# Kernel optimization log

Measured on AMD Instinct MI355X. Metric: run time of the kernel, lower is better.

The kernel has to match this reference:

```python
import jax, jax.numpy as jnp
import numpy as np

B, S, D = 4, 2048, 1024
H, DK, DV = 16, 64, 64


def setup_inputs() -> dict:
    key = jax.random.key(0)
    ks = jax.random.split(key, 9)
    std = 1.0 / np.sqrt(D)
    inp = {
        "x": jax.random.normal(ks[0], (B, S, D), jnp.float32),
        "c": jax.random.normal(ks[1], (B, S, D), jnp.float32),
        "Wq_x": jax.random.normal(ks[2], (D, H * DK), jnp.float32) * std,
        "Wk_x": jax.random.normal(ks[3], (D, H * DK), jnp.float32) * std,
        "Wv_x": jax.random.normal(ks[4], (D, H * DV), jnp.float32) * std,
        "Wq_c": jax.random.normal(ks[5], (D, H * DK), jnp.float32) * std,
        "Wk_c": jax.random.normal(ks[6], (D, H * DK), jnp.float32) * std,
        "Wv_c": jax.random.normal(ks[7], (D, H * DV), jnp.float32) * std,
        "W_proj": jax.random.normal(ks[8], (2 * H * DV, D), jnp.float32) * (1.0 / np.sqrt(2 * H * DV)),
        "b_proj": jnp.zeros((D,), jnp.float32),
    }
    return inp


def _heads(t, hd):
    # [B,S,H*hd] -> [B,H,S,hd]
    b, s, _ = t.shape
    return t.reshape(b, s, H, hd).transpose(0, 2, 1, 3)


def reference(x, c, Wq_x, Wk_x, Wv_x, Wq_c, Wk_c, Wv_c, W_proj, b_proj):
    q = jnp.concatenate([_heads(x @ Wq_x, DK), _heads(c @ Wq_c, DK)], axis=-1)  # [B,H,S,2DK]
    k = jnp.concatenate([_heads(x @ Wk_x, DK), _heads(c @ Wk_c, DK)], axis=-1)
    v = jnp.concatenate([_heads(x @ Wv_x, DV), _heads(c @ Wv_c, DV)], axis=-1)  # [B,H,S,2DV]
    # NOTE: original scales by sqrt(k_dim), not sqrt(2*k_dim) (faithful)
    scores = jnp.einsum("bhqd,bhkd->bhqk", q, k) / np.float32(np.sqrt(DK))
    attn = jax.nn.softmax(scores, axis=-1)
    out = jnp.einsum("bhqk,bhkd->bhqd", attn, v)  # [B,H,S,2DV]
    out = out.transpose(0, 2, 1, 3).reshape(x.shape[0], x.shape[1], -1)  # [B,S,H*2DV]
    return out @ W_proj + b_proj
```

## Files before the change

kernel.cpp:

```cpp
#include <hip/hip_runtime.h>
#include <hip/hip_bf16.h>
#include <stdint.h>

#define BB 4
#define SS 2048
#define DD 1024
#define HH 16
#define DHH 128

typedef __bf16 bf16x8 __attribute__((ext_vector_type(8)));
typedef __bf16 bf16x4 __attribute__((ext_vector_type(4)));
typedef float  f32x4  __attribute__((ext_vector_type(4)));
typedef short  short4v __attribute__((ext_vector_type(4)));

#define SL2E 0.180336880111186f

#if __has_builtin(__builtin_amdgcn_exp2f)
#define EXP2(x) __builtin_amdgcn_exp2f(x)
#else
#define EXP2(x) exp2f(x)
#endif

#define GLOAD_LDS16(gp, lp) \
  __builtin_amdgcn_global_load_lds((const __attribute__((address_space(1))) unsigned int*)(gp), \
                                   (__attribute__((address_space(3))) unsigned int*)(lp), 16, 0, 0)

static __device__ inline f32x4 mfma16(short4v a, short4v b, f32x4 c) {
#if __has_builtin(__builtin_amdgcn_mfma_f32_16x16x16bf16_1k)
    return __builtin_amdgcn_mfma_f32_16x16x16bf16_1k(a, b, c, 0, 0, 0);
#else
    asm volatile("v_mfma_f32_16x16x16_bf16 %0, %1, %2, %0" : "+v"(c) : "v"(a), "v"(b));
    return c;
#endif
}

static __device__ inline short4v pack4(f32x4 v) {
    bf16x4 t;
    t[0] = (__bf16)v[0]; t[1] = (__bf16)v[1]; t[2] = (__bf16)v[2]; t[3] = (__bf16)v[3];
    return __builtin_bit_cast(short4v, t);
}

__global__ void cast2_kernel(const float* __restrict__ x, const float* __restrict__ c,
                             __bf16* __restrict__ out, int n) {
    int i = (blockIdx.x * blockDim.x + threadIdx.x) * 4;
    const float* src = (i < n) ? (x + i) : (c + (i - n));
    f32x4 v = *(const f32x4*)src;
    bf16x4 o;
    o[0] = (__bf16)v[0]; o[1] = (__bf16)v[1]; o[2] = (__bf16)v[2]; o[3] = (__bf16)v[3];
    *(bf16x4*)(out + i) = o;
}

__global__ void transpose_cast_kernel(const float* __restrict__ in, __bf16* __restrict__ out,
                                      int K, int N) {
    __shared__ float tile[32][33];
    int n0 = blockIdx.x * 32, k0 = blockIdx.y * 32;
    int tx = threadIdx.x, ty = threadIdx.y;
    #pragma unroll
    for (int i = 0; i < 32; i += 8)
        tile[ty + i][tx] = in[(size_t)(k0 + ty + i) * N + n0 + tx];
    __syncthreads();
    #pragma unroll
    for (int i = 0; i < 32; i += 8)
        out[(size_t)(n0 + ty + i) * K + k0 + tx] = (__bf16)tile[tx][ty + i];
}

__global__ void transpose6_kernel(const float* s0, const float* s1, const float* s2,
                                  const float* s3, const float* s4, const float* s5,
                                  __bf16* __restrict__ dst) {
    const float* srcs[6] = {s0, s1, s2, s3, s4, s5};
    const float* __restrict__ in = srcs[blockIdx.z];
    __bf16* __restrict__ out = dst + (size_t)blockIdx.z * 1024 * 1024;
    __shared__ float tile[32][33];
    int n0 = blockIdx.x * 32, k0 = blockIdx.y * 32;
    int tx = threadIdx.x, ty = threadIdx.y;
    #pragma unroll
    for (int i = 0; i < 32; i += 8)
        tile[ty + i][tx] = in[(size_t)(k0 + ty + i) * 1024 + n0 + tx];
    __syncthreads();
    #pragma unroll
    for (int i = 0; i < 32; i += 8)
        out[(size_t)(n0 + ty + i) * 1024 + k0 + tx] = (__bf16)tile[tx][ty + i];
}

template <int EPI>
__global__ void gemm128_kernel(const __bf16* __restrict__ A0, const __bf16* __restrict__ A1,
                               const __bf16* __restrict__ B0, const __bf16* __restrict__ B1,
                               int K, void* __restrict__ outp,
                               const float* __restrict__ bias) {
    const int z = blockIdx.z;
    const __bf16* __restrict__ A  = z ? A1 : A0;
    const __bf16* __restrict__ Bt = z ? B1 : B0;
    const int qkv_off = z * 64;

    __shared__ __bf16 As[128][32];
    __shared__ __bf16 Bs[128][32];
    const int t = threadIdx.x;
    const int wave = t >> 6, lane = t & 63;
    const int l15 = lane & 15, quad = lane >> 4;
    const int wm = (wave & 1) * 64, wn = (wave >> 1) * 64;
    const int m0 = blockIdx.x * 128, n0 = blockIdx.y * 128;
    const int lrow = lane >> 2;
    const int lcol = (lane & 3) * 8;

    f32x4 acc[4][4] = {};

    for (int k0 = 0; k0 < K; k0 += 32) {
        #pragma unroll
        for (int c2 = 0; c2 < 2; ++c2) {
            int rb = (wave * 2 + c2) * 16;
            GLOAD_LDS16(A  + (size_t)(m0 + rb + lrow) * K + k0 + lcol, &As[rb][0]);
            GLOAD_LDS16(Bt + (size_t)(n0 + rb + lrow) * K + k0 + lcol, &Bs[rb][0]);
        }
        __syncthreads();
        bf16x8 af[4], bfv[4];
        #pragma unroll
        for (int i = 0; i < 4; ++i) af[i]  = *(const bf16x8*)&As[wm + i * 16 + l15][quad * 8];
        #pragma unroll
        for (int i = 0; i < 4; ++i) bfv[i] = *(const bf16x8*)&Bs[wn + i * 16 + l15][quad * 8];
        #pragma unroll
        for (int mi = 0; mi < 4; ++mi)
            #pragma unroll
            for (int ni = 0; ni < 4; ++ni)
                acc[mi][ni] = __builtin_amdgcn_mfma_f32_16x16x32_bf16(af[mi], bfv[ni], acc[mi][ni], 0, 0, 0);
        __syncthreads();
    }

    const size_t nQKV = (size_t)BB * HH * SS * DHH;
    #pragma unroll
    for (int mi = 0; mi < 4; ++mi) {
        #pragma unroll
        for (int ni = 0; ni < 4; ++ni) {
            #pragma unroll
            for (int rr = 0; rr < 4; ++rr) {
                int m = m0 + wm + mi * 16 + quad * 4 + rr;
                int n = n0 + wn + ni * 16 + l15;
                if (EPI == 1) {
                    float* o = (float*)outp;
                    o[(size_t)m * 1024 + n] = acc[mi][ni][rr] + bias[n];
                } else if (EPI == 2) {
                    int h = m >> 6, dl = m & 63;
                    int b = n >> 11, s = n & (SS - 1);
                    __bf16* vt = (__bf16*)outp;
                    vt[(((size_t)b * HH + h) * DHH + dl + qkv_off) * SS + s] = (__bf16)acc[mi][ni][rr];
                } else {
                    int b = m >> 11, s = m & (SS - 1);
                    int n1 = n & 1023;
                    int h = n1 >> 6, d = (n1 & 63) + qkv_off;
                    if (n < 1024) {
                        __bf16* q = (__bf16*)outp;
                        q[(((size_t)b * HH + h) * SS + s) * DHH + d] = (__bf16)(acc[mi][ni][rr] * SL2E);
                    } else {
                        int dsw = (((d >> 3) ^ (s & 15)) << 3) | (d & 7);
                        __bf16* kq = (__bf16*)outp + nQKV;
                        kq[(((size_t)b * HH + h) * SS + s) * DHH + dsw] = (__bf16)acc[mi][ni][rr];
                    }
                }
            }
        }
    }
}

#define LDS_VT 16384
__global__ __launch_bounds__(256, 3)
void attn_kernel(const __bf16* __restrict__ Q, const __bf16* __restrict__ Kg,
                 const __bf16* __restrict__ Vg, __bf16* __restrict__ O) {
    __shared__ __align__(16) char smem[32768];

    const int t = threadIdx.x;
    const int wave = t >> 6, lane = t & 63;
    const int l15 = lane & 15, quad = lane >> 4;
    const int bh = blockIdx.y;
    const int b = bh >> 4, h = bh & 15;
    const int mt = blockIdx.x;
    const size_t base  = (size_t)bh * SS * DHH;
    const size_t vbase = (size_t)bh * DHH * SS;

    int kaddr[4];
    #pragma unroll
    for (int kst = 0; kst < 4; ++kst)
        kaddr[kst] = l15 * 256 + (((4 * kst + quad) ^ l15) & 15) * 16;
    int vaddr[4];
    #pragma unroll
    for (int nl = 0; nl < 4; ++nl)
        vaddr[nl] = LDS_VT + l15 * 128 +
                    (((nl * 2 + (quad >> 1)) ^ (l15 & 7)) & 7) * 16 + (quad & 1) * 8;

    const __bf16* kstage = Kg + base + (size_t)wave * 2048 + lane * 8;
    const __bf16* vstage = Vg + vbase + (size_t)(wave * 32 + (lane >> 3)) * SS
                           + ((lane & 7) ^ ((lane >> 3) & 7)) * 8;

    bf16x8 qf[2][4];
    #pragma unroll
    for (int mb = 0; mb < 2; ++mb) {
        int row = mt * 128 + wave * 32 + mb * 16 + l15;
        #pragma unroll
        for (int kst = 0; kst < 4; ++kst)
            qf[mb][kst] = *(const bf16x8*)(Q + base + (size_t)row * DHH + kst * 32 + quad * 8);
    }

    f32x4 oacc[2][8] = {};
    float li_[2] = {};

    for (int kt = 0; kt < SS / 64; ++kt) {
        #pragma unroll
        for (int i = 0; i < 4; ++i)
            GLOAD_LDS16(kstage + (size_t)kt * 8192 + i * 512,
                        smem + wave * 4096 + i * 1024);
        #pragma unroll
        for (int i = 0; i < 4; ++i)
            GLOAD_LDS16(vstage + kt * 64 + (size_t)i * 8 * SS,
                        smem + LDS_VT + wave * 4096 + i * 1024);
        __syncthreads();

        f32x4 sx[2][4] = {};
        #pragma unroll
        for (int kst = 0; kst < 4; ++kst) {
            #pragma unroll
            for (int nl = 0; nl < 4; ++nl) {
                bf16x8 kf = *(const bf16x8*)(smem + kaddr[kst] + 4096 * nl);
                sx[0][nl] = __builtin_amdgcn_mfma_f32_16x16x32_bf16(kf, qf[0][kst], sx[0][nl], 0, 0, 0);
                sx[1][nl] = __builtin_amdgcn_mfma_f32_16x16x32_bf16(kf, qf[1][kst], sx[1][nl], 0, 0, 0);
            }
        }

        short4v pb[2][4];
        #pragma unroll
        for (int mb = 0; mb < 2; ++mb)
            #pragma unroll
            for (int nl = 0; nl < 4; ++nl) {
                #pragma unroll
                for (int rr = 0; rr < 4; ++rr) {
                    float p = EXP2(sx[mb][nl][rr]);
                    li_[mb] += p;
                    sx[mb][nl][rr] = p;
                }
                pb[mb][nl] = pack4(sx[mb][nl]);
            }

        #pragma unroll
        for (int nl = 0; nl < 4; ++nl) {
            #pragma unroll
            for (int ds = 0; ds < 8; ++ds) {
                short4v vf = *(const short4v*)(smem + vaddr[nl] + 2048 * ds);
                oacc[0][ds] = mfma16(vf, pb[0][nl], oacc[0][ds]);
                oacc[1][ds] = mfma16(vf, pb[1][nl], oacc[1][ds]);
            }
        }
        __syncthreads();
    }

    float inv[2];
    #pragma unroll
    for (int mb = 0; mb < 2; ++mb) {
        float v = li_[mb];
        v += __shfl_xor(v, 16);
        v += __shfl_xor(v, 32);
        inv[mb] = 1.f / v;
    }

    #pragma unroll
    for (int mb = 0; mb < 2; ++mb) {
        int mloc = wave * 32 + mb * 16 + l15;
        #pragma unroll
        for (int ds = 0; ds < 8; ++ds)
            #pragma unroll
            for (int rr = 0; rr < 4; ++rr) {
                int d = ds * 16 + quad * 4 + rr;
                int addr = mloc * 256 + (((d >> 3) ^ l15) & 15) * 16 + (d & 7) * 2;
                *(__bf16*)(smem + addr) = (__bf16)(oacc[mb][ds][rr] * inv[mb]);
            }
    }
    __syncthreads();
    #pragma unroll
    for (int i = 0; i < 8; ++i) {
        int idx = t + i * 256;
        int mloc = idx >> 4, cc = idx & 15;
        bf16x8 vv = *(const bf16x8*)(smem + mloc * 256 + ((cc ^ (mloc & 15)) & 15) * 16);
        int s = mt * 128 + mloc;
        *(bf16x8*)(O + ((size_t)b * SS + s) * (HH * DHH) + h * DHH + cc * 8) = vv;
    }
}

extern "C" void kernel_launch(void* const* d_in, const int* in_sizes, int n_in,
                              void* d_out, int out_size, void* d_ws, size_t ws_size,
                              hipStream_t stream) {
    const float* x      = (const float*)d_in[0];
    const float* c      = (const float*)d_in[1];
    const float* Wq_x   = (const float*)d_in[2];
    const float* Wk_x   = (const float*)d_in[3];
    const float* Wv_x   = (const float*)d_in[4];
    const float* Wq_c   = (const float*)d_in[5];
    const float* Wk_c   = (const float*)d_in[6];
    const float* Wv_c   = (const float*)d_in[7];
    const float* W_proj = (const float*)d_in[8];
    const float* b_proj = (const float*)d_in[9];

    const size_t nXC  = (size_t)BB * SS * DD;
    const size_t nW   = (size_t)DD * DD;
    const size_t nWP  = (size_t)(2 * HH * 64) * DD;
    const size_t nQKV = (size_t)BB * HH * SS * DHH;

    __bf16* ws  = (__bf16*)d_ws;
    __bf16* xb  = ws;
    __bf16* cb  = xb + nXC;
    __bf16* wt0 = cb + nXC;
    __bf16* wt2 = wt0 + 2 * nW;
    __bf16* wt3 = wt0 + 3 * nW;
    __bf16* wt5 = wt0 + 5 * nW;
    __bf16* wtp = wt0 + 6 * nW;
    __bf16* Qb  = wtp + nWP;
    __bf16* Kb  = Qb + nQKV;
    __bf16* Vb  = Kb + nQKV;
    __bf16* Ob  = xb;

    cast2_kernel<<<(int)(2 * nXC / 1024), 256, 0, stream>>>(x, c, xb, (int)nXC);

    transpose6_kernel<<<dim3(32, 32, 6), dim3(32, 8), 0, stream>>>(
        Wq_x, Wk_x, Wv_x, Wq_c, Wk_c, Wv_c, wt0);
    transpose_cast_kernel<<<dim3(32, 64), dim3(32, 8), 0, stream>>>(W_proj, wtp, 2048, 1024);

    gemm128_kernel<4><<<dim3(64, 16, 2), 256, 0, stream>>>(xb, cb, wt0, wt3, 1024, Qb, nullptr);
    gemm128_kernel<2><<<dim3(8, 64, 2), 256, 0, stream>>>(wt2, wt5, xb, cb, 1024, Vb, nullptr);

    attn_kernel<<<dim3(16, 64), 256, 0, stream>>>(Qb, Kb, Vb, Ob);

    gemm128_kernel<1><<<dim3(64, 8, 1), 256, 0, stream>>>(Ob, nullptr, wtp, nullptr, 2048, d_out, b_proj);
}
```

Baseline: 494.7 us.

## Fuse QKV projections into one GEMM with LDS-staged vectorized epilogue stores

Merges the separate Q/K and V projection GEMMs into a single launch covering all three outputs (N grid 24 tiles), with V written transposed from the normal layout via an LDS-staged swizzled tile. The epilogue now stages each wave's accumulators in shared memory and issues 16-byte vector stores instead of scattered 2-byte stores. The weight transposes are also merged into one launch, including both halves of W_proj. This removes launch overhead and uncoalesced epilogue writes, at the cost of extra LDS traffic and more complex indexing.

```diff
diff --git a/kernel.cpp b/kernel.cpp
--- a/kernel.cpp
+++ b/kernel.cpp
@@ -50,36 +50,27 @@
     *(bf16x4*)(out + i) = o;
 }
 
-__global__ void transpose_cast_kernel(const float* __restrict__ in, __bf16* __restrict__ out,
-                                      int K, int N) {
+__global__ void transpose8_kernel(const float* s0, const float* s1, const float* s2,
+                                  const float* s3, const float* s4, const float* s5,
+                                  const float* sp, __bf16* __restrict__ wt0,
+                                  __bf16* __restrict__ wtp) {
+    const int z = blockIdx.z;
+    const float* srcs[8] = {s0, s1, s2, s3, s4, s5, sp, sp + 1024 * 1024};
+    const float* __restrict__ in = srcs[z];
+    __bf16* __restrict__ out = (z < 6) ? (wt0 + (size_t)z * 1024 * 1024) : wtp;
+    const int ostride = (z < 6) ? 1024 : 2048;
+    const int koff    = (z < 7) ? 0 : 1024;
+
     __shared__ float tile[32][33];
     int n0 = blockIdx.x * 32, k0 = blockIdx.y * 32;
     int tx = threadIdx.x, ty = threadIdx.y;
     #pragma unroll
     for (int i = 0; i < 32; i += 8)
-        tile[ty + i][tx] = in[(size_t)(k0 + ty + i) * N + n0 + tx];
-    __syncthreads();
-    #pragma unroll
-    for (int i = 0; i < 32; i += 8)
-        out[(size_t)(n0 + ty + i) * K + k0 + tx] = (__bf16)tile[tx][ty + i];
-}
-
-__global__ void transpose6_kernel(const float* s0, const float* s1, const float* s2,
-                                  const float* s3, const float* s4, const float* s5,
-                                  __bf16* __restrict__ dst) {
-    const float* srcs[6] = {s0, s1, s2, s3, s4, s5};
-    const float* __restrict__ in = srcs[blockIdx.z];
-    __bf16* __restrict__ out = dst + (size_t)blockIdx.z * 1024 * 1024;
-    __shared__ float tile[32][33];
-    int n0 = blockIdx.x * 32, k0 = blockIdx.y * 32;
-    int tx = threadIdx.x, ty = threadIdx.y;
-    #pragma unroll
-    for (int i = 0; i < 32; i += 8)
         tile[ty + i][tx] = in[(size_t)(k0 + ty + i) * 1024 + n0 + tx];
     __syncthreads();
     #pragma unroll
     for (int i = 0; i < 32; i += 8)
-        out[(size_t)(n0 + ty + i) * 1024 + k0 + tx] = (__bf16)tile[tx][ty + i];
+        out[(size_t)(n0 + ty + i) * ostride + koff + k0 + tx] = (__bf16)tile[tx][ty + i];
 }
 
 template <int EPI>
@@ -92,8 +83,10 @@
     const __bf16* __restrict__ Bt = z ? B1 : B0;
     const int qkv_off = z * 64;
 
-    __shared__ __bf16 As[128][32];
-    __shared__ __bf16 Bs[128][32];
+    __shared__ __align__(16) char gsm[16384];
+    __bf16 (*As)[32] = (__bf16 (*)[32])gsm;
+    __bf16 (*Bs)[32] = (__bf16 (*)[32])(gsm + 8192);
+
     const int t = threadIdx.x;
     const int wave = t >> 6, lane = t & 63;
     const int l15 = lane & 15, quad = lane >> 4;
@@ -126,35 +119,93 @@
     }
 
     const size_t nQKV = (size_t)BB * HH * SS * DHH;
-    #pragma unroll
-    for (int mi = 0; mi < 4; ++mi) {
-        #pragma unroll
-        for (int ni = 0; ni < 4; ++ni) {
-            #pragma unroll
-            for (int rr = 0; rr < 4; ++rr) {
-                int m = m0 + wm + mi * 16 + quad * 4 + rr;
-                int n = n0 + wn + ni * 16 + l15;
-                if (EPI == 1) {
+
+    if (EPI == 1) {
+        #pragma unroll
+        for (int mi = 0; mi < 4; ++mi)
+            #pragma unroll
+            for (int ni = 0; ni < 4; ++ni)
+                #pragma unroll
+                for (int rr = 0; rr < 4; ++rr) {
+                    int m = m0 + wm + mi * 16 + quad * 4 + rr;
+                    int n = n0 + wn + ni * 16 + l15;
                     float* o = (float*)outp;
                     o[(size_t)m * 1024 + n] = acc[mi][ni][rr] + bias[n];
-                } else if (EPI == 2) {
-                    int h = m >> 6, dl = m & 63;
-                    int b = n >> 11, s = n & (SS - 1);
-                    __bf16* vt = (__bf16*)outp;
-                    vt[(((size_t)b * HH + h) * DHH + dl + qkv_off) * SS + s] = (__bf16)acc[mi][ni][rr];
-                } else {
-                    int b = m >> 11, s = m & (SS - 1);
-                    int n1 = n & 1023;
-                    int h = n1 >> 6, d = (n1 & 63) + qkv_off;
-                    if (n < 1024) {
-                        __bf16* q = (__bf16*)outp;
-                        q[(((size_t)b * HH + h) * SS + s) * DHH + d] = (__bf16)(acc[mi][ni][rr] * SL2E);
-                    } else {
-                        int dsw = (((d >> 3) ^ (s & 15)) << 3) | (d & 7);
-                        __bf16* kq = (__bf16*)outp + nQKV;
-                        kq[(((size_t)b * HH + h) * SS + s) * DHH + dsw] = (__bf16)acc[mi][ni][rr];
+                }
+        return;
+    }
+
+    char* reg = gsm + wave * 4096;
+    const int path = (n0 + wn) >> 10;
+
+    #pragma unroll
+    for (int np = 0; np < 2; ++np) {
+        if (path < 2) {
+            #pragma unroll
+            for (int mi = 0; mi < 4; ++mi)
+                #pragma unroll
+                for (int nn = 0; nn < 2; ++nn) {
+                    int ni = np * 2 + nn;
+                    #pragma unroll
+                    for (int rr = 0; rr < 4; ++rr) {
+                        int ml = mi * 16 + quad * 4 + rr, nl = nn * 16 + l15;
+                        float v = acc[mi][ni][rr];
+                        if (path == 0) v *= SL2E;
+                        *(__bf16*)(reg + ml * 64 + nl * 2) = (__bf16)v;
                     }
                 }
+        } else {
+            #pragma unroll
+            for (int mi = 0; mi < 4; ++mi)
+                #pragma unroll
+                for (int nn = 0; nn < 2; ++nn) {
+                    int ni = np * 2 + nn;
+                    #pragma unroll
+                    for (int rr = 0; rr < 4; ++rr) {
+                        int ml = mi * 16 + quad * 4 + rr, nl = nn * 16 + l15;
+                        int ad = nl * 128 + ((((ml >> 3) ^ (nl & 7)) & 7) * 16) + (ml & 7) * 2;
+                        *(__bf16*)(reg + ad) = (__bf16)acc[mi][ni][rr];
+                    }
+                }
+        }
+        int nbase = n0 + wn + np * 32;
+        if (path == 0) {
+            __bf16* q = (__bf16*)outp;
+            #pragma unroll
+            for (int i = 0; i < 4; ++i) {
+                int ml = i * 16 + (lane >> 2), ng = (lane & 3) * 8;
+                bf16x8 v = *(const bf16x8*)(reg + ml * 64 + ng * 2);
+                int m = m0 + wm + ml;
+                int b = m >> 11, s = m & (SS - 1);
+                int n1 = (nbase + ng) & 1023;
+                int h = n1 >> 6, d = (n1 & 63) + qkv_off;
+                *(bf16x8*)(q + (((size_t)b * HH + h) * SS + s) * DHH + d) = v;
+            }
+        } else if (path == 1) {
+            __bf16* kq = (__bf16*)outp + nQKV;
+            #pragma unroll
+            for (int i = 0; i < 4; ++i) {
+                int ml = i * 16 + (lane >> 2), ng = (lane & 3) * 8;
+                bf16x8 v = *(const bf16x8*)(reg + ml * 64 + ng * 2);
+                int m = m0 + wm + ml;
+                int b = m >> 11, s = m & (SS - 1);
+                int n1 = (nbase + ng) & 1023;
+                int h = n1 >> 6, d = (n1 & 63) + qkv_off;
+                int dsw = (((d >> 3) ^ (s & 15)) << 3);
+                *(bf16x8*)(kq + (((size_t)b * HH + h) * SS + s) * DHH + dsw) = v;
+            }
+        } else {
+            __bf16* vt = (__bf16*)outp + 2 * nQKV;
+            #pragma unroll
+            for (int i = 0; i < 4; ++i) {
+                int dl = i * 8 + (lane >> 3), sg = (lane & 7) * 8;
+                int chunk = ((lane & 7) ^ (dl & 7)) & 7;
+                bf16x8 v = *(const bf16x8*)(reg + dl * 128 + chunk * 16);
+                int n2 = (nbase + dl) & 1023;
+                int h = n2 >> 6, d = (n2 & 63) + qkv_off;
+                int m = m0 + wm + sg;
+                int b = m >> 11, s = m & (SS - 1);
+                *(bf16x8*)(vt + (((size_t)b * HH + h) * DHH + d) * SS + s) = v;
             }
         }
     }
@@ -304,9 +355,7 @@
     __bf16* xb  = ws;
     __bf16* cb  = xb + nXC;
     __bf16* wt0 = cb + nXC;
-    __bf16* wt2 = wt0 + 2 * nW;
     __bf16* wt3 = wt0 + 3 * nW;
-    __bf16* wt5 = wt0 + 5 * nW;
     __bf16* wtp = wt0 + 6 * nW;
     __bf16* Qb  = wtp + nWP;
     __bf16* Kb  = Qb + nQKV;
@@ -315,12 +364,10 @@
 
     cast2_kernel<<<(int)(2 * nXC / 1024), 256, 0, stream>>>(x, c, xb, (int)nXC);
 
-    transpose6_kernel<<<dim3(32, 32, 6), dim3(32, 8), 0, stream>>>(
-        Wq_x, Wk_x, Wv_x, Wq_c, Wk_c, Wv_c, wt0);
-    transpose_cast_kernel<<<dim3(32, 64), dim3(32, 8), 0, stream>>>(W_proj, wtp, 2048, 1024);
-
-    gemm128_kernel<4><<<dim3(64, 16, 2), 256, 0, stream>>>(xb, cb, wt0, wt3, 1024, Qb, nullptr);
-    gemm128_kernel<2><<<dim3(8, 64, 2), 256, 0, stream>>>(wt2, wt5, xb, cb, 1024, Vb, nullptr);
+    transpose8_kernel<<<dim3(32, 32, 8), dim3(32, 8), 0, stream>>>(
+        Wq_x, Wk_x, Wv_x, Wq_c, Wk_c, Wv_c, W_proj, wt0, wtp);
+
+    gemm128_kernel<5><<<dim3(64, 24, 2), 256, 0, stream>>>(xb, cb, wt0, wt3, 1024, Qb, nullptr);
 
     attn_kernel<<<dim3(16, 64), 256, 0, stream>>>(Qb, Kb, Vb, Ob);
 
```

Result: no change. 488.5 us (-1.3%).
